# Performance work log

Hardware: AMD Instinct MI355X
Metric: run time of the kernel (lower is better)

## Reference

```python
import jax, jax.numpy as jnp
import numpy as np

EPS = 1e-5
NEG_SLOPE = 0.2
B, C, P, K, E, H = 16, 16, 2048, 16, 64, 2


def cross_set_gather(f, idx):
    # f: (B, C, P), idx: (B, P, K) -> (B, C, P, K)
    return jax.vmap(lambda fb, ib: fb[:, ib])(f, idx)


def bn(x, g, b, m, v, axes):
    # x normalized along channel dim; g,b,m,v shaped to broadcast via `axes` reshape
    return (x - m.reshape(axes)) * (g.reshape(axes) / jnp.sqrt(v.reshape(axes) + EPS)) + b.reshape(axes)


def setup_inputs() -> dict:
    key = jax.random.key(0)
    ks = jax.random.split(key, 16)
    features = jax.random.normal(ks[0], (B, C, P), dtype=jnp.float32)
    neighbor_indices = jax.random.randint(ks[1], (B, P, K), 0, P)
    mask = jax.random.randint(ks[2], (B, 1, P), 0, 2).astype(bool)
    s = 0.1
    return {
        "features": features,
        "neighbor_indices": neighbor_indices,
        "mask": mask,
        "node_w": jax.random.normal(ks[3], (H, E, C)) * s,
        "node_g": jnp.ones((H, E)),
        "node_b": jnp.zeros((H, E)),
        "node_m": jax.random.normal(ks[4], (H, E)) * s,
        "node_v": jax.random.uniform(ks[5], (H, E)) + 0.5,
        "edge_w": jax.random.normal(ks[6], (H, E, C)) * s,
        "edge_bias": jax.random.normal(ks[7], (H, E)) * s,
        "edge_g": jnp.ones((H, E)),
        "edge_b2": jnp.zeros((H, E)),
        "edge_m": jax.random.normal(ks[8], (H, E)) * s,
        "edge_v": jax.random.uniform(ks[9], (H, E)) + 0.5,
        "self_w": jax.random.normal(ks[10], (H, E)) * s,
        "self_b": jax.random.normal(ks[11], (H,)) * s,
        "nb_w": jax.random.normal(ks[12], (H, E)) * s,
        "nb_b": jax.random.normal(ks[13], (H,)) * s,
    }


def _forward(features, neighbor_indices, mask, node_w, node_g, node_b, node_m, node_v,
             edge_w, edge_bias, edge_g, edge_b2, edge_m, edge_v, self_w, self_b, nb_w, nb_b):
    mask_f = mask.astype(features.dtype)  # (B,1,P)
    # node encoding (Conv1d k=1 + BN): (B,H,E,P)
    nodes = jnp.einsum('hec,bcp->bhep', node_w, features)
    nodes = bn(nodes, node_g, node_b, node_m, node_v, (1, H, E, 1))
    # edge features: neighbor - center, (B,C,P,K)
    nbr = cross_set_gather(features, neighbor_indices)
    edge_feat = nbr - features[:, :, :, None]
    # edge encoding (Conv2d k=1 + BN): (B,H,E,P,K)
    enc = jnp.einsum('hec,bcpk->bhepk', edge_w, edge_feat) + edge_bias[None, :, :, None, None]
    enc = bn(enc, edge_g, edge_b2, edge_m, edge_v, (1, H, E, 1, 1))
    # attention scores
    self_score = jnp.einsum('he,bhep->bhp', self_w, nodes) + self_b[None, :, None]  # (B,H,P)
    nb_score = jnp.einsum('he,bhepk->bhpk', nb_w, enc) + nb_b[None, :, None, None]  # (B,H,P,K)
    logits = self_score[..., None] + nb_score
    logits = jnp.where(logits >= 0, logits, NEG_SLOPE * logits)  # leaky_relu(0.2)
    # neighbor validity mask: (B,P,K)
    valid = cross_set_gather(mask_f, neighbor_indices)[:, 0]
    vb = valid[:, None, :, :]  # (B,1,P,K)
    logits = jnp.where(vb == 0, -jnp.inf, logits)
    coef = jnp.nan_to_num(jax.nn.softmax(logits, axis=-1), nan=0.0, posinf=0.0, neginf=0.0)  # (B,H,P,K)
    # weighted aggregation + relu: (B,H,E,P)
    att = jax.nn.relu(jnp.einsum('bhpk,bhepk->bhep', coef, enc))
    # graph features: masked max over K
    enc_masked = jnp.where(vb[:, :, None, :, :] == 0, -jnp.inf, enc)
    graph = jnp.max(enc_masked, axis=-1)  # (B,H,E,P)
    graph = jnp.where(jnp.isinf(graph), 0.0, graph)
    # multi-head combine: element-wise max over heads, then mask
    att_out = jnp.max(att, axis=1) * mask_f  # (B,E,P)
    graph_out = jnp.max(graph, axis=1) * mask_f  # (B,E,P)
    return att_out, graph_out


def reference(features, neighbor_indices, mask, node_w, node_g, node_b, node_m, node_v,
              edge_w, edge_bias, edge_g, edge_b2, edge_m, edge_v, self_w, self_b, nb_w, nb_b):
    return _forward(features, neighbor_indices, mask, node_w, node_g, node_b, node_m, node_v,
                    edge_w, edge_bias, edge_g, edge_b2, edge_m, edge_v, self_w, self_b, nb_w, nb_b)
```

## Files before the change

### kernel.cpp

```cpp
#include <hip/hip_runtime.h>
#include <hip/hip_bf16.h>
#include <math.h>

#define NB 16
#define NC 16
#define NP 2048
#define NK 16
#define NE 64
#define NH 2
#define EPSV 1e-5f
#define NSLOPE 0.2f
#define QINV -1e30f
#define QTHR -1e29f

#define WS_PINFO   16384
#define WS_EPROJ   544768

__device__ __forceinline__ float ldf(const void* p, int i, int isb) {
  return isb ? __bfloat162float(((const __hip_bfloat16*)p)[i]) : ((const float*)p)[i];
}

__global__ void __launch_bounds__(256) k_proj(
    const void* feat, const void* mask,
    const void* edge_w, const void* node_w,
    const void* edge_g, const void* edge_v, const void* edge_bias,
    const void* edge_m, const void* edge_b2,
    const void* node_g, const void* node_v, const void* node_b, const void* node_m,
    const void* self_w, const void* self_b, const void* nb_w,
    char* ws)
{
  __shared__ int sh_isb, sh_mbyte;
  __shared__ float ewl[128*17];
  __shared__ float nwl[128*17];
  __shared__ float fl[NC][64];
  __shared__ float w2[128], wn[128], ctr[128];
  __shared__ float s_wq[32], s_wsc[32], s_cself[2];

  const int tid = threadIdx.x;
  const int w = tid >> 6, lane = tid & 63;

  if (w == 0) {
    const unsigned short* u = (const unsigned short*)feat;
    int cnt = 0;
#pragma unroll
    for (int i = 0; i < 8; i++) {
      int ex = (u[lane*8 + i] >> 7) & 0xFF;
      cnt += (ex >= 100 && ex <= 135) ? 1 : 0;
    }
#pragma unroll
    for (int o = 32; o >= 1; o >>= 1) cnt += __shfl_xor(cnt, o);
    if (lane == 0) sh_isb = (cnt >= 460) ? 1 : 0;
  }
  if (w == 1) {
    const unsigned char* mb = (const unsigned char*)mask;
    int c = 0;
#pragma unroll
    for (int i = 0; i < 16; i++) {
      int ix = lane*16 + i;
      c += ((ix & 3) && mb[ix]) ? 1 : 0;
    }
#pragma unroll
    for (int o = 32; o >= 1; o >>= 1) c += __shfl_xor(c, o);
    if (lane == 0) sh_mbyte = (c > 0) ? 1 : 0;
  }
  __syncthreads();
  const int isb = sh_isb, mbyte = sh_mbyte;

  const int bid = blockIdx.x;
  const int b  = (bid & 7) * 2 + ((bid >> 3) & 1);
  const int pt = bid >> 4;
  const int p0 = pt * 64;

  for (int i = tid; i < NH*NE*NC; i += 256) {
    const int he = i >> 4, c = i & 15;
    ewl[he*17 + c] = ldf(edge_w, i, isb);
    nwl[he*17 + c] = ldf(node_w, i, isb);
  }
  for (int i = tid; i < NC*64; i += 256) {
    int c = i >> 6, p = i & 63;
    fl[c][p] = ldf(feat, (b*NC + c)*NP + p0 + p, isb);
  }
  if (tid < 128) {
    const int he = tid;
    float se = ldf(edge_g, he, isb) * rsqrtf(ldf(edge_v, he, isb) + EPSV);
    float ns = ldf(node_g, he, isb) * rsqrtf(ldf(node_v, he, isb) + EPSV);
    w2[he]  = ldf(nb_w, he, isb) * se;
    wn[he]  = ldf(self_w, he, isb) * ns;
    ctr[he] = ldf(self_w, he, isb) * (ldf(node_b, he, isb) - ldf(node_m, he, isb) * ns);
  }
  __syncthreads();
  if (tid < NH*NC) {
    const int h = tid >> 4, c = tid & 15;
    float sq = 0.f, sn = 0.f;
#pragma unroll 8
    for (int e = 0; e < NE; e++) {
      sq += w2[h*NE+e] * ewl[(h*NE+e)*17 + c];
      sn += wn[h*NE+e] * nwl[(h*NE+e)*17 + c];
    }
    s_wq[tid]  = sq;
    s_wsc[tid] = sn;
  }
  if (tid < NH) {
    float cs = 0.f;
#pragma unroll 8
    for (int e = 0; e < NE; e++) cs += ctr[tid*NE+e];
    s_cself[tid] = cs + ldf(self_b, tid, isb);
  }
  __syncthreads();

  const int c2 = tid & 127;
  const int e = c2 >> 1, h = c2 & 1;
  const int ph = tid >> 7;
  float wv[NC];
#pragma unroll
  for (int c = 0; c < NC; c++) wv[c] = ewl[(h*NE + e)*17 + c];

  float* eo = (float*)(ws + WS_EPROJ);
  const long base = (long)(b*NP + p0) * 128;
  for (int i = 0; i < 32; i++) {
    const int p = i*2 + ph;
    float acc = 0.f;
#pragma unroll
    for (int c = 0; c < NC; c++) acc = fmaf(wv[c], fl[c][p], acc);
    eo[base + (long)p*128 + c2] = acc;
  }

  if (tid < 64) {
    float q0=0.f, q1=0.f, s0=0.f, s1=0.f;
#pragma unroll
    for (int c = 0; c < NC; c++) {
      const float f = fl[c][tid];
      q0 = fmaf(s_wq[c],      f, q0);
      q1 = fmaf(s_wq[NC+c],   f, q1);
      s0 = fmaf(s_wsc[c],     f, s0);
      s1 = fmaf(s_wsc[NC+c],  f, s1);
    }
    const int p = p0 + tid;
    bool mv;
    if (mbyte) mv = ((const unsigned char*)mask)[b*NP + p] != 0;
    else       mv = ((const int*)mask)[b*NP + p] != 0;
    float4 pi;
    pi.x = mv ? q0 : QINV;
    pi.y = mv ? q1 : QINV;
    pi.z = s0 + s_cself[0];
    pi.w = s1 + s_cself[1];
    ((float4*)(ws + WS_PINFO))[b*NP + p] = pi;
  }
}

__global__ void __launch_bounds__(256, 4) k_main(
    const void* feat, const int* nidx,
    const void* edge_g, const void* edge_v, const void* edge_bias,
    const void* edge_m, const void* edge_b2,
    const void* nb_w, const void* nb_b,
    char* ws, void* out)
{
  __shared__ int sh_isb;
  __shared__ float sh_se[128], sh_cbe[128], sh_cnb[2];
  __shared__ float2 c01[4][8][NK];
  __shared__ int    idxc[4][8][NK];
  __shared__ unsigned char s_cnt[4][8], s_cm[4][8];
  __shared__ float att_t[NE][33];
  __shared__ float gr_t[NE][33];

  const int tid  = threadIdx.x;
  const int w    = tid >> 6;
  const int lane = tid & 63;

  if (w == 0) {
    const unsigned short* u = (const unsigned short*)feat;
    int cnt = 0;
#pragma unroll
    for (int i = 0; i < 8; i++) {
      int ex = (u[lane*8 + i] >> 7) & 0xFF;
      cnt += (ex >= 100 && ex <= 135) ? 1 : 0;
    }
#pragma unroll
    for (int o = 32; o >= 1; o >>= 1) cnt += __shfl_xor(cnt, o);
    if (lane == 0) sh_isb = (cnt >= 460) ? 1 : 0;
  }
  __syncthreads();
  const int isb = sh_isb;

  if (tid < 128) {
    const int he = tid, h = tid >> 6;
    float se = ldf(edge_g, he, isb) * rsqrtf(ldf(edge_v, he, isb) + EPSV);
    float cb = se * (ldf(edge_bias, he, isb) - ldf(edge_m, he, isb)) + ldf(edge_b2, he, isb);
    sh_se[he]  = se;
    sh_cbe[he] = cb;
    float t = ldf(nb_w, he, isb) * cb;
#pragma unroll
    for (int o = 32; o >= 1; o >>= 1) t += __shfl_xor(t, o);
    if ((tid & 63) == 0) sh_cnb[h] = t + ldf(nb_b, h, isb);
  }
  __syncthreads();

  const float4* pinfo = (const float4*)(ws + WS_PINFO);
  const float2* ep2   = (const float2*)(ws + WS_EPROJ);

  const int bid = blockIdx.x;
  const int b  = (bid & 7) * 2 + ((bid >> 3) & 1);
  const int pt = bid >> 4;
  const int p0 = pt * 32;
  const int jj = lane >> 4, kk = lane & 15;
  const float cnb0 = sh_cnb[0], cnb1 = sh_cnb[1];

  for (int jr = 0; jr < 2; jr++) {
    const int pw4 = p0 + w*8 + jr*4;
    const int idx_l = nidx[(b*NP + pw4)*NK + lane];
    const float4 P  = pinfo[b*NP + idx_l];
    const float4 Pc = pinfo[b*NP + pw4 + jj];
    const bool valid = (P.x > QTHR);
    const unsigned long long vm = __ballot(valid);
    const unsigned vmj = (unsigned)((vm >> (16*jj)) & 0xFFFFull);
    const bool anyv = (vmj != 0);

    float c0, c1;
    {
      float l0 = Pc.z + P.x - Pc.x + cnb0;
      l0 = (l0 >= 0.f) ? l0 : NSLOPE * l0;
      float mx = l0;
#pragma unroll
      for (int o = 8; o >= 1; o >>= 1) mx = fmaxf(mx, __shfl_xor(mx, o));
      float ex = __expf(l0 - mx);
      float sm = ex;
#pragma unroll
      for (int o = 8; o >= 1; o >>= 1) sm += __shfl_xor(sm, o);
      c0 = anyv ? ex / sm : 0.f;
    }
    {
      float l1 = Pc.w + P.y - Pc.y + cnb1;
      l1 = (l1 >= 0.f) ? l1 : NSLOPE * l1;
      float mx = l1;
#pragma unroll
      for (int o = 8; o >= 1; o >>= 1) mx = fmaxf(mx, __shfl_xor(mx, o));
      float ex = __expf(l1 - mx);
      float sm = ex;
#pragma unroll
      for (int o = 8; o >= 1; o >>= 1) sm += __shfl_xor(sm, o);
      c1 = anyv ? ex / sm : 0.f;
    }
    const int jx = jr*4 + jj;
    const int pos = __popc(vmj & ((1u << kk) - 1));
    if (valid) {
      c01[w][jx][pos]  = make_float2(c0, c1);
      idxc[w][jx][pos] = idx_l;
    }
    if (kk == 0) {
      s_cnt[w][jx] = (unsigned char)__popc(vmj);
      s_cm[w][jx]  = (Pc.x > QTHR) ? 1 : 0;
    }
  }

  const float se0 = sh_se[lane],  se1 = sh_se[NE + lane];
  const float cb0 = sh_cbe[lane], cb1 = sh_cbe[NE + lane];
  const long rowb = (long)b * NP;

  for (int j = 0; j < 8; j++) {
    const int pj = p0 + w*8 + j;
    const int pl = w*8 + j;
    if (!s_cm[w][j]) { att_t[lane][pl] = 0.f; gr_t[lane][pl] = 0.f; continue; }
    const int cnt = s_cnt[w][j];
    const float2 rawc = ep2[(rowb + pj)*NE + lane];
    const float cpe0 = cb0 - se0*rawc.x, cpe1 = cb1 - se1*rawc.y;

    float a0 = 0.f, a1 = 0.f;
    float mx0 = -INFINITY, mn0 = INFINITY, mx1 = -INFINITY, mn1 = INFINITY;
#pragma unroll 4
    for (int k = 0; k < cnt; k++) {
      const float2 cf = c01[w][j][k];
      const int ix = idxc[w][j][k];
      const float2 v = ep2[(rowb + ix)*NE + lane];
      a0 = fmaf(cf.x, v.x, a0);
      a1 = fmaf(cf.y, v.y, a1);
      mx0 = fmaxf(mx0, v.x); mn0 = fminf(mn0, v.x);
      mx1 = fmaxf(mx1, v.y); mn1 = fminf(mn1, v.y);
    }
    const bool av = (cnt > 0);
    const float csel = av ? 1.f : 0.f;
    const float att0 = fmaxf(fmaf(se0, a0, cpe0*csel), 0.f);
    const float att1 = fmaxf(fmaf(se1, a1, cpe1*csel), 0.f);
    const float g0 = av ? (((se0 >= 0.f) ? se0*mx0 : se0*mn0) + cpe0) : 0.f;
    const float g1 = av ? (((se1 >= 0.f) ? se1*mx1 : se1*mn1) + cpe1) : 0.f;
    att_t[lane][pl] = fmaxf(att0, att1);
    gr_t[lane][pl]  = fmaxf(g0, g1);
  }
  __syncthreads();

  const long obase = (long)b * NE * NP;
  for (int i = tid; i < NE*32; i += 256) {
    const int ee = i >> 5, pp = i & 31;
    const long oi = obase + (long)ee * NP + p0 + pp;
    const float av = att_t[ee][pp], gv = gr_t[ee][pp];
    if (isb) {
      ((__hip_bfloat16*)out)[oi] = __float2bfloat16(av);
      ((__hip_bfloat16*)out)[oi + (long)NB*NE*NP] = __float2bfloat16(gv);
    } else {
      ((float*)out)[oi] = av;
      ((float*)out)[oi + (long)NB*NE*NP] = gv;
    }
  }
}

extern "C" void kernel_launch(void* const* d_in, const int* in_sizes, int n_in,
                              void* d_out, int out_size, void* d_ws, size_t ws_size,
                              hipStream_t stream)
{
  const void* feat      = d_in[0];
  const void* nidx      = d_in[1];
  const void* mask      = d_in[2];
  const void* node_w    = d_in[3];
  const void* node_g    = d_in[4];
  const void* node_b    = d_in[5];
  const void* node_m    = d_in[6];
  const void* node_v    = d_in[7];
  const void* edge_w    = d_in[8];
  const void* edge_bias = d_in[9];
  const void* edge_g    = d_in[10];
  const void* edge_b2   = d_in[11];
  const void* edge_m    = d_in[12];
  const void* edge_v    = d_in[13];
  const void* self_w    = d_in[14];
  const void* self_b    = d_in[15];
  const void* nb_w      = d_in[16];
  const void* nb_b      = d_in[17];
  char* ws = (char*)d_ws;

  hipLaunchKernelGGL(k_proj, dim3(NB*(NP/64)), dim3(256), 0, stream,
                     feat, mask, edge_w, node_w,
                     edge_g, edge_v, edge_bias, edge_m, edge_b2,
                     node_g, node_v, node_b, node_m,
                     self_w, self_b, nb_w, ws);
  hipLaunchKernelGGL(k_main, dim3(NB*(NP/32)), dim3(256), 0, stream,
                     feat, (const int*)nidx,
                     edge_g, edge_v, edge_bias, edge_m, edge_b2,
                     nb_w, nb_b, ws, d_out);
}
```

Baseline: 129.1 us.

## Split into pinfo/coef/gather kernels with LDS-resident bf16 edge projections

Restructures the pipeline into three kernels. Per-point coefficients and neighbor indices are compacted into a global workspace. Each gather block then recomputes a 4-channel slice of the edge projection for the whole batch row into LDS as bf16, so the neighbor gathers read LDS instead of a large global fp32 projection buffer. Coefficients are stored as fp16. This reduces global memory traffic from the random gathers, but adds redundant projection recompute per channel slice, lowers precision, and uses large LDS per block, which limits occupancy.

```diff
diff --git a/kernel.cpp b/kernel.cpp
--- a/kernel.cpp
+++ b/kernel.cpp
@@ -1,5 +1,6 @@
 #include <hip/hip_runtime.h>
 #include <hip/hip_bf16.h>
+#include <hip/hip_fp16.h>
 #include <math.h>
 
 #define NB 16
@@ -13,26 +14,30 @@
 #define QINV -1e30f
 #define QTHR -1e29f
 
-#define WS_PINFO   16384
-#define WS_EPROJ   544768
+#define WS_PINFO 16384
+#define WS_ENT   540672
+#define WS_CNT   4734976
 
 __device__ __forceinline__ float ldf(const void* p, int i, int isb) {
   return isb ? __bfloat162float(((const __hip_bfloat16*)p)[i]) : ((const float*)p)[i];
 }
-
-__global__ void __launch_bounds__(256) k_proj(
+__device__ __forceinline__ unsigned f2bf(float f) {
+  unsigned u = __float_as_uint(f);
+  return (u + 0x7FFFu + ((u >> 16) & 1u)) >> 16;
+}
+__device__ __forceinline__ float bflo(unsigned v) { return __uint_as_float(v << 16); }
+__device__ __forceinline__ float bfhi(unsigned v) { return __uint_as_float(v & 0xFFFF0000u); }
+
+__global__ void __launch_bounds__(256) k_pinfo(
     const void* feat, const void* mask,
     const void* edge_w, const void* node_w,
-    const void* edge_g, const void* edge_v, const void* edge_bias,
-    const void* edge_m, const void* edge_b2,
+    const void* edge_g, const void* edge_v,
     const void* node_g, const void* node_v, const void* node_b, const void* node_m,
     const void* self_w, const void* self_b, const void* nb_w,
     char* ws)
 {
   __shared__ int sh_isb, sh_mbyte;
-  __shared__ float ewl[128*17];
-  __shared__ float nwl[128*17];
-  __shared__ float fl[NC][64];
+  __shared__ float ewl[128*17], nwl[128*17];
   __shared__ float w2[128], wn[128], ctr[128];
   __shared__ float s_wq[32], s_wsc[32], s_cself[2];
 
@@ -66,19 +71,10 @@
   __syncthreads();
   const int isb = sh_isb, mbyte = sh_mbyte;
 
-  const int bid = blockIdx.x;
-  const int b  = (bid & 7) * 2 + ((bid >> 3) & 1);
-  const int pt = bid >> 4;
-  const int p0 = pt * 64;
-
-  for (int i = tid; i < NH*NE*NC; i += 256) {
+  for (int i = tid; i < 128*16; i += 256) {
     const int he = i >> 4, c = i & 15;
     ewl[he*17 + c] = ldf(edge_w, i, isb);
     nwl[he*17 + c] = ldf(node_w, i, isb);
-  }
-  for (int i = tid; i < NC*64; i += 256) {
-    int c = i >> 6, p = i & 63;
-    fl[c][p] = ldf(feat, (b*NC + c)*NP + p0 + p, isb);
   }
   if (tid < 128) {
     const int he = tid;
@@ -89,7 +85,7 @@
     ctr[he] = ldf(self_w, he, isb) * (ldf(node_b, he, isb) - ldf(node_m, he, isb) * ns);
   }
   __syncthreads();
-  if (tid < NH*NC) {
+  if (tid < 32) {
     const int h = tid >> 4, c = tid & 15;
     float sq = 0.f, sn = 0.f;
 #pragma unroll 8
@@ -100,7 +96,7 @@
     s_wq[tid]  = sq;
     s_wsc[tid] = sn;
   }
-  if (tid < NH) {
+  if (tid < 2) {
     float cs = 0.f;
 #pragma unroll 8
     for (int e = 0; e < NE; e++) cs += ctr[tid*NE+e];
@@ -108,64 +104,42 @@
   }
   __syncthreads();
 
-  const int c2 = tid & 127;
-  const int e = c2 >> 1, h = c2 & 1;
-  const int ph = tid >> 7;
-  float wv[NC];
-#pragma unroll
-  for (int c = 0; c < NC; c++) wv[c] = ewl[(h*NE + e)*17 + c];
-
-  float* eo = (float*)(ws + WS_EPROJ);
-  const long base = (long)(b*NP + p0) * 128;
-  for (int i = 0; i < 32; i++) {
-    const int p = i*2 + ph;
-    float acc = 0.f;
-#pragma unroll
-    for (int c = 0; c < NC; c++) acc = fmaf(wv[c], fl[c][p], acc);
-    eo[base + (long)p*128 + c2] = acc;
-  }
-
-  if (tid < 64) {
-    float q0=0.f, q1=0.f, s0=0.f, s1=0.f;
-#pragma unroll
-    for (int c = 0; c < NC; c++) {
-      const float f = fl[c][tid];
-      q0 = fmaf(s_wq[c],      f, q0);
-      q1 = fmaf(s_wq[NC+c],   f, q1);
-      s0 = fmaf(s_wsc[c],     f, s0);
-      s1 = fmaf(s_wsc[NC+c],  f, s1);
-    }
-    const int p = p0 + tid;
-    bool mv;
-    if (mbyte) mv = ((const unsigned char*)mask)[b*NP + p] != 0;
-    else       mv = ((const int*)mask)[b*NP + p] != 0;
-    float4 pi;
-    pi.x = mv ? q0 : QINV;
-    pi.y = mv ? q1 : QINV;
-    pi.z = s0 + s_cself[0];
-    pi.w = s1 + s_cself[1];
-    ((float4*)(ws + WS_PINFO))[b*NP + p] = pi;
-  }
-}
-
-__global__ void __launch_bounds__(256, 4) k_main(
+  const int bid = blockIdx.x;
+  const int b = (bid & 7)*2 + ((bid >> 3) & 1);
+  const int chunk = bid >> 4;
+  const int p = chunk*256 + w*64 + lane;
+
+  float q0=0.f, q1=0.f, s0=0.f, s1=0.f;
+#pragma unroll
+  for (int c = 0; c < NC; c++) {
+    const float fc = ldf(feat, (b*NC + c)*NP + p, isb);
+    q0 = fmaf(s_wq[c],     fc, q0);
+    q1 = fmaf(s_wq[16+c],  fc, q1);
+    s0 = fmaf(s_wsc[c],    fc, s0);
+    s1 = fmaf(s_wsc[16+c], fc, s1);
+  }
+  bool mv;
+  if (mbyte) mv = ((const unsigned char*)mask)[b*NP + p] != 0;
+  else       mv = ((const int*)mask)[b*NP + p] != 0;
+  float4 pi;
+  pi.x = mv ? q0 : QINV;
+  pi.y = mv ? q1 : QINV;
+  pi.z = s0 + s_cself[0];
+  pi.w = s1 + s_cself[1];
+  ((float4*)(ws + WS_PINFO))[b*NP + p] = pi;
+}
+
+__global__ void __launch_bounds__(256) k_coef(
     const void* feat, const int* nidx,
     const void* edge_g, const void* edge_v, const void* edge_bias,
     const void* edge_m, const void* edge_b2,
     const void* nb_w, const void* nb_b,
-    char* ws, void* out)
+    char* ws)
 {
   __shared__ int sh_isb;
-  __shared__ float sh_se[128], sh_cbe[128], sh_cnb[2];
-  __shared__ float2 c01[4][8][NK];
-  __shared__ int    idxc[4][8][NK];
-  __shared__ unsigned char s_cnt[4][8], s_cm[4][8];
-  __shared__ float att_t[NE][33];
-  __shared__ float gr_t[NE][33];
-
-  const int tid  = threadIdx.x;
-  const int w    = tid >> 6;
-  const int lane = tid & 63;
+  __shared__ float sh_cnb[2];
+  const int tid = threadIdx.x;
+  const int w = tid >> 6, lane = tid & 63;
 
   if (w == 0) {
     const unsigned short* u = (const unsigned short*)feat;
@@ -186,8 +160,6 @@
     const int he = tid, h = tid >> 6;
     float se = ldf(edge_g, he, isb) * rsqrtf(ldf(edge_v, he, isb) + EPSV);
     float cb = se * (ldf(edge_bias, he, isb) - ldf(edge_m, he, isb)) + ldf(edge_b2, he, isb);
-    sh_se[he]  = se;
-    sh_cbe[he] = cb;
     float t = ldf(nb_w, he, isb) * cb;
 #pragma unroll
     for (int o = 32; o >= 1; o >>= 1) t += __shfl_xor(t, o);
@@ -196,20 +168,20 @@
   __syncthreads();
 
   const float4* pinfo = (const float4*)(ws + WS_PINFO);
-  const float2* ep2   = (const float2*)(ws + WS_EPROJ);
+  uint2* ent = (uint2*)(ws + WS_ENT);
+  unsigned char* cntg = (unsigned char*)(ws + WS_CNT);
 
   const int bid = blockIdx.x;
-  const int b  = (bid & 7) * 2 + ((bid >> 3) & 1);
-  const int pt = bid >> 4;
-  const int p0 = pt * 32;
+  const int b = (bid & 7)*2 + ((bid >> 3) & 1);
+  const int chunk = bid >> 4;
   const int jj = lane >> 4, kk = lane & 15;
   const float cnb0 = sh_cnb[0], cnb1 = sh_cnb[1];
 
-  for (int jr = 0; jr < 2; jr++) {
-    const int pw4 = p0 + w*8 + jr*4;
-    const int idx_l = nidx[(b*NP + pw4)*NK + lane];
+  for (int s = 0; s < 16; s++) {
+    const int p4 = chunk*256 + w*64 + s*4;
+    const int idx_l = nidx[(b*NP + p4)*NK + lane];
     const float4 P  = pinfo[b*NP + idx_l];
-    const float4 Pc = pinfo[b*NP + pw4 + jj];
+    const float4 Pc = pinfo[b*NP + p4 + jj];
     const bool valid = (P.x > QTHR);
     const unsigned long long vm = __ballot(valid);
     const unsigned vmj = (unsigned)((vm >> (16*jj)) & 0xFFFFull);
@@ -240,64 +212,162 @@
       for (int o = 8; o >= 1; o >>= 1) sm += __shfl_xor(sm, o);
       c1 = anyv ? ex / sm : 0.f;
     }
-    const int jx = jr*4 + jj;
     const int pos = __popc(vmj & ((1u << kk) - 1));
     if (valid) {
-      c01[w][jx][pos]  = make_float2(c0, c1);
-      idxc[w][jx][pos] = idx_l;
+      __half2 h2 = __floats2half2_rn(c0, c1);
+      uint2 e;
+      e.x = *(unsigned*)&h2;
+      e.y = (unsigned)idx_l;
+      ent[(long)(b*NP + p4 + jj)*NK + pos] = e;
     }
     if (kk == 0) {
-      s_cnt[w][jx] = (unsigned char)__popc(vmj);
-      s_cm[w][jx]  = (Pc.x > QTHR) ? 1 : 0;
-    }
-  }
-
-  const float se0 = sh_se[lane],  se1 = sh_se[NE + lane];
-  const float cb0 = sh_cbe[lane], cb1 = sh_cbe[NE + lane];
-  const long rowb = (long)b * NP;
-
-  for (int j = 0; j < 8; j++) {
-    const int pj = p0 + w*8 + j;
-    const int pl = w*8 + j;
-    if (!s_cm[w][j]) { att_t[lane][pl] = 0.f; gr_t[lane][pl] = 0.f; continue; }
-    const int cnt = s_cnt[w][j];
-    const float2 rawc = ep2[(rowb + pj)*NE + lane];
-    const float cpe0 = cb0 - se0*rawc.x, cpe1 = cb1 - se1*rawc.y;
-
-    float a0 = 0.f, a1 = 0.f;
-    float mx0 = -INFINITY, mn0 = INFINITY, mx1 = -INFINITY, mn1 = INFINITY;
-#pragma unroll 4
-    for (int k = 0; k < cnt; k++) {
-      const float2 cf = c01[w][j][k];
-      const int ix = idxc[w][j][k];
-      const float2 v = ep2[(rowb + ix)*NE + lane];
-      a0 = fmaf(cf.x, v.x, a0);
-      a1 = fmaf(cf.y, v.y, a1);
-      mx0 = fmaxf(mx0, v.x); mn0 = fminf(mn0, v.x);
-      mx1 = fmaxf(mx1, v.y); mn1 = fminf(mn1, v.y);
-    }
-    const bool av = (cnt > 0);
+      const int cm = (Pc.x > QTHR) ? 0x80 : 0;
+      cntg[b*NP + p4 + jj] = (unsigned char)(__popc(vmj) | cm);
+    }
+  }
+}
+
+__global__ void __launch_bounds__(256) k_gather(
+    const void* feat, const void* edge_w,
+    const void* edge_g, const void* edge_v, const void* edge_bias,
+    const void* edge_m, const void* edge_b2,
+    char* ws, void* out)
+{
+  __shared__ int sh_isb;
+  __shared__ unsigned epl[NP*4];
+  __shared__ uint2 entw[4][32][17];
+  __shared__ float wzl[8*16];
+  __shared__ float secb[16];
+
+  const int tid = threadIdx.x;
+  const int w = tid >> 6, lane = tid & 63;
+
+  if (w == 0) {
+    const unsigned short* u = (const unsigned short*)feat;
+    int cnt = 0;
+#pragma unroll
+    for (int i = 0; i < 8; i++) {
+      int ex = (u[lane*8 + i] >> 7) & 0xFF;
+      cnt += (ex >= 100 && ex <= 135) ? 1 : 0;
+    }
+#pragma unroll
+    for (int o = 32; o >= 1; o >>= 1) cnt += __shfl_xor(cnt, o);
+    if (lane == 0) sh_isb = (cnt >= 460) ? 1 : 0;
+  }
+  __syncthreads();
+  const int isb = sh_isb;
+
+  const int bid = blockIdx.x;
+  const int b  = (bid & 7)*2 + ((bid >> 3) & 1);
+  const int r  = bid >> 4;
+  const int ec = r & 15;
+  const int ph = r >> 4;
+
+  if (tid < 128) {
+    const int u = tid >> 4, c = tid & 15;
+    const int e = u >> 1, h = u & 1;
+    wzl[u*16 + c] = ldf(edge_w, (h*NE + ec*4 + e)*NC + c, isb);
+  }
+  if (tid < 8) {
+    const int e = tid >> 1, h = tid & 1;
+    const int he = h*NE + ec*4 + e;
+    float se = ldf(edge_g, he, isb) * rsqrtf(ldf(edge_v, he, isb) + EPSV);
+    float cb = se * (ldf(edge_bias, he, isb) - ldf(edge_m, he, isb)) + ldf(edge_b2, he, isb);
+    secb[tid]     = se;
+    secb[8 + tid] = cb;
+  }
+  __syncthreads();
+
+  for (int t = w; t < 32; t += 4) {
+    const int p = t*64 + lane;
+    float acc[8] = {0.f,0.f,0.f,0.f,0.f,0.f,0.f,0.f};
+#pragma unroll
+    for (int c = 0; c < NC; c++) {
+      const float fc = ldf(feat, (b*NC + c)*NP + p, isb);
+#pragma unroll
+      for (int u = 0; u < 8; u++) acc[u] = fmaf(wzl[u*16 + c], fc, acc[u]);
+    }
+    uint4 pk;
+    pk.x = f2bf(acc[0]) | (f2bf(acc[1]) << 16);
+    pk.y = f2bf(acc[2]) | (f2bf(acc[3]) << 16);
+    pk.z = f2bf(acc[4]) | (f2bf(acc[5]) << 16);
+    pk.w = f2bf(acc[6]) | (f2bf(acc[7]) << 16);
+    *(uint4*)&epl[p*4] = pk;
+  }
+  __syncthreads();
+
+  const int u = lane >> 5, pi = lane & 31;
+  const float sea0 = secb[u*4 + 0], sea1 = secb[u*4 + 1];
+  const float seb0 = secb[u*4 + 2], seb1 = secb[u*4 + 3];
+  const float cba0 = secb[8 + u*4 + 0], cba1 = secb[8 + u*4 + 1];
+  const float cbb0 = secb[8 + u*4 + 2], cbb1 = secb[8 + u*4 + 3];
+
+  const uint4* entg = (const uint4*)(ws + WS_ENT);
+  const unsigned char* cntg = (const unsigned char*)(ws + WS_CNT);
+  const long go = (long)NB * NE * NP;
+
+  for (int g = 0; g < 8; g++) {
+    const int pg = ph*1024 + w*256 + g*32;
+    const long eb4 = (long)(b*NP + pg) * 8;
+#pragma unroll
+    for (int ps = 0; ps < 4; ps++) {
+      const int li4 = ps*64 + lane;
+      const uint4 v = entg[eb4 + li4];
+      const int pl = li4 >> 3, k0 = (li4 & 7) * 2;
+      entw[w][pl][k0]     = make_uint2(v.x, v.y);
+      entw[w][pl][k0 + 1] = make_uint2(v.z, v.w);
+    }
+    const unsigned cc = cntg[b*NP + pg + pi];
+    const int cnte = (cc & 0x80) ? (int)(cc & 0x7F) : 0;
+
+    const uint2 ce = *(const uint2*)&epl[(pg + pi)*4 + u*2];
+    const float ra0 = bflo(ce.x), ra1 = bfhi(ce.x);
+    const float rb0 = bflo(ce.y), rb1 = bfhi(ce.y);
+    const float cpa0 = cba0 - sea0*ra0, cpa1 = cba1 - sea1*ra1;
+    const float cpb0 = cbb0 - seb0*rb0, cpb1 = cbb1 - seb1*rb1;
+
+    float aa0=0.f, aa1=0.f, ab0=0.f, ab1=0.f;
+    float mxa0=-INFINITY, mna0=INFINITY, mxa1=-INFINITY, mna1=INFINITY;
+    float mxb0=-INFINITY, mnb0=INFINITY, mxb1=-INFINITY, mnb1=INFINITY;
+    for (int k = 0; k < cnte; k++) {
+      const uint2 en = entw[w][pi][k];
+      const __half2 hc = *(const __half2*)&en.x;
+      const float c0 = __low2float(hc), c1 = __high2float(hc);
+      const uint2 pv = *(const uint2*)&epl[en.y*4 + u*2];
+      const float va0 = bflo(pv.x), va1 = bfhi(pv.x);
+      const float vb0 = bflo(pv.y), vb1 = bfhi(pv.y);
+      aa0 = fmaf(c0, va0, aa0); aa1 = fmaf(c1, va1, aa1);
+      ab0 = fmaf(c0, vb0, ab0); ab1 = fmaf(c1, vb1, ab1);
+      mxa0 = fmaxf(mxa0, va0); mna0 = fminf(mna0, va0);
+      mxa1 = fmaxf(mxa1, va1); mna1 = fminf(mna1, va1);
+      mxb0 = fmaxf(mxb0, vb0); mnb0 = fminf(mnb0, vb0);
+      mxb1 = fmaxf(mxb1, vb1); mnb1 = fminf(mnb1, vb1);
+    }
+    const bool av = (cnte > 0);
     const float csel = av ? 1.f : 0.f;
-    const float att0 = fmaxf(fmaf(se0, a0, cpe0*csel), 0.f);
-    const float att1 = fmaxf(fmaf(se1, a1, cpe1*csel), 0.f);
-    const float g0 = av ? (((se0 >= 0.f) ? se0*mx0 : se0*mn0) + cpe0) : 0.f;
-    const float g1 = av ? (((se1 >= 0.f) ? se1*mx1 : se1*mn1) + cpe1) : 0.f;
-    att_t[lane][pl] = fmaxf(att0, att1);
-    gr_t[lane][pl]  = fmaxf(g0, g1);
-  }
-  __syncthreads();
-
-  const long obase = (long)b * NE * NP;
-  for (int i = tid; i < NE*32; i += 256) {
-    const int ee = i >> 5, pp = i & 31;
-    const long oi = obase + (long)ee * NP + p0 + pp;
-    const float av = att_t[ee][pp], gv = gr_t[ee][pp];
+    const float ta0 = fmaxf(fmaf(sea0, aa0, cpa0*csel), 0.f);
+    const float ta1 = fmaxf(fmaf(sea1, aa1, cpa1*csel), 0.f);
+    const float tb0 = fmaxf(fmaf(seb0, ab0, cpb0*csel), 0.f);
+    const float tb1 = fmaxf(fmaf(seb1, ab1, cpb1*csel), 0.f);
+    const float atta = fmaxf(ta0, ta1);
+    const float attb = fmaxf(tb0, tb1);
+    const float ga0 = av ? fmaf(sea0, (sea0 >= 0.f) ? mxa0 : mna0, cpa0) : 0.f;
+    const float ga1 = av ? fmaf(sea1, (sea1 >= 0.f) ? mxa1 : mna1, cpa1) : 0.f;
+    const float gb0 = av ? fmaf(seb0, (seb0 >= 0.f) ? mxb0 : mnb0, cpb0) : 0.f;
+    const float gb1 = av ? fmaf(seb1, (seb1 >= 0.f) ? mxb1 : mnb1, cpb1) : 0.f;
+    const float gra = fmaxf(ga0, ga1);
+    const float grb = fmaxf(gb0, gb1);
+
+    const long oa = (long)(b*NE + ec*4 + u*2) * NP + pg + pi;
+    const long ob = oa + NP;
     if (isb) {
-      ((__hip_bfloat16*)out)[oi] = __float2bfloat16(av);
-      ((__hip_bfloat16*)out)[oi + (long)NB*NE*NP] = __float2bfloat16(gv);
+      __hip_bfloat16* o = (__hip_bfloat16*)out;
+      o[oa] = __float2bfloat16(atta);  o[ob] = __float2bfloat16(attb);
+      o[oa + go] = __float2bfloat16(gra); o[ob + go] = __float2bfloat16(grb);
     } else {
-      ((float*)out)[oi] = av;
-      ((float*)out)[oi + (long)NB*NE*NP] = gv;
+      float* o = (float*)out;
+      o[oa] = atta;  o[ob] = attb;
+      o[oa + go] = gra; o[ob + go] = grb;
     }
   }
 }
@@ -326,13 +396,17 @@
   const void* nb_b      = d_in[17];
   char* ws = (char*)d_ws;
 
-  hipLaunchKernelGGL(k_proj, dim3(NB*(NP/64)), dim3(256), 0, stream,
+  hipLaunchKernelGGL(k_pinfo, dim3(128), dim3(256), 0, stream,
                      feat, mask, edge_w, node_w,
-                     edge_g, edge_v, edge_bias, edge_m, edge_b2,
+                     edge_g, edge_v,
                      node_g, node_v, node_b, node_m,
                      self_w, self_b, nb_w, ws);
-  hipLaunchKernelGGL(k_main, dim3(NB*(NP/32)), dim3(256), 0, stream,
+  hipLaunchKernelGGL(k_coef, dim3(128), dim3(256), 0, stream,
                      feat, (const int*)nidx,
                      edge_g, edge_v, edge_bias, edge_m, edge_b2,
-                     nb_w, nb_b, ws, d_out);
-}
+                     nb_w, nb_b, ws);
+  hipLaunchKernelGGL(k_gather, dim3(512), dim3(256), 0, stream,
+                     feat, edge_w,
+                     edge_g, edge_v, edge_bias, edge_m, edge_b2,
+                     ws, d_out);
+}
```

Measured after the change: 145.5 us. +12.7%, slower.

## Store edge projections as packed bf16 and compute softmax per-thread serially

Applied to the files above, without the earlier changes.

The intermediate edge projection buffer now holds packed bf16 pairs instead of fp32, halving the bytes written by k_proj and gathered per neighbor in k_main. Softmax coefficients are computed by 32 threads, each handling a whole point with vectorized index loads, and stored compactly as half2 coefficients with precomputed byte offsets. The launch-bounds occupancy hint is removed. This trades accuracy (bf16 projections, fp16 logits and coefficients) for lower memory traffic, and the serial softmax stage uses only half of one wave while the other waves wait at the barrier.

```diff
diff --git a/kernel.cpp b/kernel.cpp
--- a/kernel.cpp
+++ b/kernel.cpp
@@ -1,5 +1,6 @@
 #include <hip/hip_runtime.h>
 #include <hip/hip_bf16.h>
+#include <hip/hip_fp16.h>
 #include <math.h>
 
 #define NB 16
@@ -13,18 +14,23 @@
 #define QINV -1e30f
 #define QTHR -1e29f
 
-#define WS_PINFO   16384
-#define WS_EPROJ   544768
+#define WS_PINFO 16384
+#define WS_EPB   2162688
 
 __device__ __forceinline__ float ldf(const void* p, int i, int isb) {
   return isb ? __bfloat162float(((const __hip_bfloat16*)p)[i]) : ((const float*)p)[i];
 }
+__device__ __forceinline__ unsigned f2bf(float f) {
+  unsigned u = __float_as_uint(f);
+  return (u + 0x7FFFu + ((u >> 16) & 1u)) >> 16;
+}
+__device__ __forceinline__ float bflo(unsigned v) { return __uint_as_float(v << 16); }
+__device__ __forceinline__ float bfhi(unsigned v) { return __uint_as_float(v & 0xFFFF0000u); }
 
 __global__ void __launch_bounds__(256) k_proj(
     const void* feat, const void* mask,
     const void* edge_w, const void* node_w,
-    const void* edge_g, const void* edge_v, const void* edge_bias,
-    const void* edge_m, const void* edge_b2,
+    const void* edge_g, const void* edge_v,
     const void* node_g, const void* node_v, const void* node_b, const void* node_m,
     const void* self_w, const void* self_b, const void* nb_w,
     char* ws)
@@ -67,11 +73,11 @@
   const int isb = sh_isb, mbyte = sh_mbyte;
 
   const int bid = blockIdx.x;
-  const int b  = (bid & 7) * 2 + ((bid >> 3) & 1);
+  const int b  = (bid & 7)*2 + ((bid >> 3) & 1);
   const int pt = bid >> 4;
   const int p0 = pt * 64;
 
-  for (int i = tid; i < NH*NE*NC; i += 256) {
+  for (int i = tid; i < 128*16; i += 256) {
     const int he = i >> 4, c = i & 15;
     ewl[he*17 + c] = ldf(edge_w, i, isb);
     nwl[he*17 + c] = ldf(node_w, i, isb);
@@ -89,7 +95,7 @@
     ctr[he] = ldf(self_w, he, isb) * (ldf(node_b, he, isb) - ldf(node_m, he, isb) * ns);
   }
   __syncthreads();
-  if (tid < NH*NC) {
+  if (tid < 32) {
     const int h = tid >> 4, c = tid & 15;
     float sq = 0.f, sn = 0.f;
 #pragma unroll 8
@@ -100,7 +106,7 @@
     s_wq[tid]  = sq;
     s_wsc[tid] = sn;
   }
-  if (tid < NH) {
+  if (tid < 2) {
     float cs = 0.f;
 #pragma unroll 8
     for (int e = 0; e < NE; e++) cs += ctr[tid*NE+e];
@@ -108,21 +114,26 @@
   }
   __syncthreads();
 
-  const int c2 = tid & 127;
-  const int e = c2 >> 1, h = c2 & 1;
-  const int ph = tid >> 7;
-  float wv[NC];
-#pragma unroll
-  for (int c = 0; c < NC; c++) wv[c] = ewl[(h*NE + e)*17 + c];
-
-  float* eo = (float*)(ws + WS_EPROJ);
-  const long base = (long)(b*NP + p0) * 128;
-  for (int i = 0; i < 32; i++) {
-    const int p = i*2 + ph;
-    float acc = 0.f;
-#pragma unroll
-    for (int c = 0; c < NC; c++) acc = fmaf(wv[c], fl[c][p], acc);
-    eo[base + (long)p*128 + c2] = acc;
+  const int e = tid & 63;
+  const int pp = tid >> 6;
+  float wv0[NC], wv1[NC];
+#pragma unroll
+  for (int c = 0; c < NC; c++) {
+    wv0[c] = ewl[e*17 + c];
+    wv1[c] = ewl[(NE + e)*17 + c];
+  }
+  unsigned* epb = (unsigned*)(ws + WS_EPB);
+  const long base = (long)(b*NP + p0) * 64;
+  for (int pass = 0; pass < 16; pass++) {
+    const int p = pass*4 + pp;
+    float a0 = 0.f, a1 = 0.f;
+#pragma unroll
+    for (int c = 0; c < NC; c++) {
+      const float f = fl[c][p];
+      a0 = fmaf(wv0[c], f, a0);
+      a1 = fmaf(wv1[c], f, a1);
+    }
+    epb[base + (long)p*64 + e] = f2bf(a0) | (f2bf(a1) << 16);
   }
 
   if (tid < 64) {
@@ -130,10 +141,10 @@
 #pragma unroll
     for (int c = 0; c < NC; c++) {
       const float f = fl[c][tid];
-      q0 = fmaf(s_wq[c],      f, q0);
-      q1 = fmaf(s_wq[NC+c],   f, q1);
-      s0 = fmaf(s_wsc[c],     f, s0);
-      s1 = fmaf(s_wsc[NC+c],  f, s1);
+      q0 = fmaf(s_wq[c],     f, q0);
+      q1 = fmaf(s_wq[16+c],  f, q1);
+      s0 = fmaf(s_wsc[c],    f, s0);
+      s1 = fmaf(s_wsc[16+c], f, s1);
     }
     const int p = p0 + tid;
     bool mv;
@@ -148,7 +159,7 @@
   }
 }
 
-__global__ void __launch_bounds__(256, 4) k_main(
+__global__ void __launch_bounds__(256) k_main(
     const void* feat, const int* nidx,
     const void* edge_g, const void* edge_v, const void* edge_bias,
     const void* edge_m, const void* edge_b2,
@@ -157,9 +168,8 @@
 {
   __shared__ int sh_isb;
   __shared__ float sh_se[128], sh_cbe[128], sh_cnb[2];
-  __shared__ float2 c01[4][8][NK];
-  __shared__ int    idxc[4][8][NK];
-  __shared__ unsigned char s_cnt[4][8], s_cm[4][8];
+  __shared__ uint2 ent[32][17];
+  __shared__ unsigned char cntcm[32];
   __shared__ float att_t[NE][33];
   __shared__ float gr_t[NE][33];
 
@@ -196,108 +206,122 @@
   __syncthreads();
 
   const float4* pinfo = (const float4*)(ws + WS_PINFO);
-  const float2* ep2   = (const float2*)(ws + WS_EPROJ);
-
   const int bid = blockIdx.x;
-  const int b  = (bid & 7) * 2 + ((bid >> 3) & 1);
+  const int b  = (bid & 7)*2 + ((bid >> 3) & 1);
   const int pt = bid >> 4;
   const int p0 = pt * 32;
-  const int jj = lane >> 4, kk = lane & 15;
-  const float cnb0 = sh_cnb[0], cnb1 = sh_cnb[1];
-
-  for (int jr = 0; jr < 2; jr++) {
-    const int pw4 = p0 + w*8 + jr*4;
-    const int idx_l = nidx[(b*NP + pw4)*NK + lane];
-    const float4 P  = pinfo[b*NP + idx_l];
-    const float4 Pc = pinfo[b*NP + pw4 + jj];
-    const bool valid = (P.x > QTHR);
-    const unsigned long long vm = __ballot(valid);
-    const unsigned vmj = (unsigned)((vm >> (16*jj)) & 0xFFFFull);
-    const bool anyv = (vmj != 0);
-
-    float c0, c1;
+
+  if (w == 0 && lane < 32) {
+    const int p = p0 + lane;
+    const float cnb0 = sh_cnb[0], cnb1 = sh_cnb[1];
+    const float4 Pc = pinfo[b*NP + p];
+    const bool cm = (Pc.x > QTHR);
+
+    int idx[NK];
     {
+      const int4* n4 = (const int4*)(nidx + ((long)b*NP + p)*NK);
+#pragma unroll
+      for (int q = 0; q < 4; q++) {
+        const int4 v = n4[q];
+        idx[q*4+0] = v.x; idx[q*4+1] = v.y; idx[q*4+2] = v.z; idx[q*4+3] = v.w;
+      }
+    }
+    __half2 lgp[NK];
+    unsigned vmask = 0;
+    float mx0 = -INFINITY, mx1 = -INFINITY;
+#pragma unroll
+    for (int k = 0; k < NK; k++) {
+      const float2 P = *(const float2*)&pinfo[b*NP + idx[k]];
+      const bool valid = (P.x > QTHR);
       float l0 = Pc.z + P.x - Pc.x + cnb0;
       l0 = (l0 >= 0.f) ? l0 : NSLOPE * l0;
-      float mx = l0;
-#pragma unroll
-      for (int o = 8; o >= 1; o >>= 1) mx = fmaxf(mx, __shfl_xor(mx, o));
-      float ex = __expf(l0 - mx);
-      float sm = ex;
-#pragma unroll
-      for (int o = 8; o >= 1; o >>= 1) sm += __shfl_xor(sm, o);
-      c0 = anyv ? ex / sm : 0.f;
-    }
-    {
-      float l1 = Pc.w + P.y - Pc.y + cnb1;
+      float l1 = Pc.w + P.y - Pc.w + cnb1;
+      l1 = Pc.w + P.y - Pc.y + cnb1;
       l1 = (l1 >= 0.f) ? l1 : NSLOPE * l1;
-      float mx = l1;
-#pragma unroll
-      for (int o = 8; o >= 1; o >>= 1) mx = fmaxf(mx, __shfl_xor(mx, o));
-      float ex = __expf(l1 - mx);
-      float sm = ex;
-#pragma unroll
-      for (int o = 8; o >= 1; o >>= 1) sm += __shfl_xor(sm, o);
-      c1 = anyv ? ex / sm : 0.f;
-    }
-    const int jx = jr*4 + jj;
-    const int pos = __popc(vmj & ((1u << kk) - 1));
-    if (valid) {
-      c01[w][jx][pos]  = make_float2(c0, c1);
-      idxc[w][jx][pos] = idx_l;
-    }
-    if (kk == 0) {
-      s_cnt[w][jx] = (unsigned char)__popc(vmj);
-      s_cm[w][jx]  = (Pc.x > QTHR) ? 1 : 0;
-    }
-  }
+      l0 = valid ? l0 : -INFINITY;
+      l1 = valid ? l1 : -INFINITY;
+      vmask |= (valid ? 1u : 0u) << k;
+      lgp[k] = __floats2half2_rn(l0, l1);
+      mx0 = fmaxf(mx0, l0);
+      mx1 = fmaxf(mx1, l1);
+    }
+    float sm0 = 0.f, sm1 = 0.f;
+#pragma unroll
+    for (int k = 0; k < NK; k++) {
+      const float2 l = __half22float2(lgp[k]);
+      sm0 += __expf(l.x - mx0);
+      sm1 += __expf(l.y - mx1);
+    }
+    const float inv0 = 1.f / sm0, inv1 = 1.f / sm1;
+    int pos = 0;
+#pragma unroll
+    for (int k = 0; k < NK; k++) {
+      if ((vmask >> k) & 1) {
+        const float2 l = __half22float2(lgp[k]);
+        const float c0 = __expf(l.x - mx0) * inv0;
+        const float c1 = __expf(l.y - mx1) * inv1;
+        const __half2 h2 = __floats2half2_rn(c0, c1);
+        uint2 e;
+        e.x = *(const unsigned*)&h2;
+        e.y = ((unsigned)idx[k]) << 8;
+        ent[lane][pos] = e;
+        pos++;
+      }
+    }
+    cntcm[lane] = (unsigned char)(pos | (cm ? 0x80 : 0));
+  }
+  __syncthreads();
 
   const float se0 = sh_se[lane],  se1 = sh_se[NE + lane];
   const float cb0 = sh_cbe[lane], cb1 = sh_cbe[NE + lane];
-  const long rowb = (long)b * NP;
+  const char* epb_b = ws + WS_EPB + (long)b * NP * 256;
 
   for (int j = 0; j < 8; j++) {
-    const int pj = p0 + w*8 + j;
     const int pl = w*8 + j;
-    if (!s_cm[w][j]) { att_t[lane][pl] = 0.f; gr_t[lane][pl] = 0.f; continue; }
-    const int cnt = s_cnt[w][j];
-    const float2 rawc = ep2[(rowb + pj)*NE + lane];
-    const float cpe0 = cb0 - se0*rawc.x, cpe1 = cb1 - se1*rawc.y;
+    const unsigned cc = cntcm[pl];
+    if (!(cc & 0x80)) { att_t[lane][pl] = 0.f; gr_t[lane][pl] = 0.f; continue; }
+    const int cnt = cc & 0x7F;
+
+    const unsigned rawp = *(const unsigned*)(epb_b + (long)(p0 + pl)*256 + lane*4);
+    const float ra0 = bflo(rawp), ra1 = bfhi(rawp);
+    const float cpe0 = cb0 - se0*ra0, cpe1 = cb1 - se1*ra1;
 
     float a0 = 0.f, a1 = 0.f;
     float mx0 = -INFINITY, mn0 = INFINITY, mx1 = -INFINITY, mn1 = INFINITY;
 #pragma unroll 4
     for (int k = 0; k < cnt; k++) {
-      const float2 cf = c01[w][j][k];
-      const int ix = idxc[w][j][k];
-      const float2 v = ep2[(rowb + ix)*NE + lane];
-      a0 = fmaf(cf.x, v.x, a0);
-      a1 = fmaf(cf.y, v.y, a1);
-      mx0 = fmaxf(mx0, v.x); mn0 = fminf(mn0, v.x);
-      mx1 = fmaxf(mx1, v.y); mn1 = fminf(mn1, v.y);
+      const uint2 en = ent[pl][k];
+      const float2 cf = __half22float2(*(const __half2*)&en.x);
+      const unsigned v = *(const unsigned*)(epb_b + en.y + lane*4);
+      const float v0 = bflo(v), v1 = bfhi(v);
+      a0 = fmaf(cf.x, v0, a0);
+      a1 = fmaf(cf.y, v1, a1);
+      mx0 = fmaxf(mx0, v0); mn0 = fminf(mn0, v0);
+      mx1 = fmaxf(mx1, v1); mn1 = fminf(mn1, v1);
     }
     const bool av = (cnt > 0);
     const float csel = av ? 1.f : 0.f;
     const float att0 = fmaxf(fmaf(se0, a0, cpe0*csel), 0.f);
     const float att1 = fmaxf(fmaf(se1, a1, cpe1*csel), 0.f);
-    const float g0 = av ? (((se0 >= 0.f) ? se0*mx0 : se0*mn0) + cpe0) : 0.f;
-    const float g1 = av ? (((se1 >= 0.f) ? se1*mx1 : se1*mn1) + cpe1) : 0.f;
+    const float g0 = av ? fmaf(se0, (se0 >= 0.f) ? mx0 : mn0, cpe0) : 0.f;
+    const float g1 = av ? fmaf(se1, (se1 >= 0.f) ? mx1 : mn1, cpe1) : 0.f;
     att_t[lane][pl] = fmaxf(att0, att1);
     gr_t[lane][pl]  = fmaxf(g0, g1);
   }
   __syncthreads();
 
   const long obase = (long)b * NE * NP;
+  const long go = (long)NB * NE * NP;
   for (int i = tid; i < NE*32; i += 256) {
     const int ee = i >> 5, pp = i & 31;
     const long oi = obase + (long)ee * NP + p0 + pp;
     const float av = att_t[ee][pp], gv = gr_t[ee][pp];
     if (isb) {
       ((__hip_bfloat16*)out)[oi] = __float2bfloat16(av);
-      ((__hip_bfloat16*)out)[oi + (long)NB*NE*NP] = __float2bfloat16(gv);
+      ((__hip_bfloat16*)out)[oi + go] = __float2bfloat16(gv);
     } else {
       ((float*)out)[oi] = av;
-      ((float*)out)[oi + (long)NB*NE*NP] = gv;
+      ((float*)out)[oi + go] = gv;
     }
   }
 }
@@ -328,7 +352,7 @@
 
   hipLaunchKernelGGL(k_proj, dim3(NB*(NP/64)), dim3(256), 0, stream,
                      feat, mask, edge_w, node_w,
-                     edge_g, edge_v, edge_bias, edge_m, edge_b2,
+                     edge_g, edge_v,
                      node_g, node_v, node_b, node_m,
                      self_w, self_b, nb_w, ws);
   hipLaunchKernelGGL(k_main, dim3(NB*(NP/32)), dim3(256), 0, stream,
```

Result: faster. 122.7 us (-5.0%).
